# Optimization experiments

Measured on AMD Instinct MI355X. Metric: run time of the kernel, lower is better.

## Reference

```python
import jax, jax.numpy as jnp
import numpy as np

B, S, D_MODEL = 2, 2048, 1024
NUM_HEADS, ATTN_DIM = 16, 64


def setup_inputs() -> dict:
    key = jax.random.key(0)
    ks = jax.random.split(key, 9)
    scale = 1.0 / np.sqrt(D_MODEL)
    states = jax.random.normal(ks[0], (B, S, D_MODEL), dtype=jnp.float32)
    Wq = jax.random.normal(ks[1], (D_MODEL, NUM_HEADS * ATTN_DIM), dtype=jnp.float32) * scale
    bq = jnp.zeros((NUM_HEADS * ATTN_DIM,), dtype=jnp.float32)
    Wk = jax.random.normal(ks[2], (D_MODEL, NUM_HEADS * ATTN_DIM), dtype=jnp.float32) * scale
    bk = jnp.zeros((NUM_HEADS * ATTN_DIM,), dtype=jnp.float32)
    Wv = jax.random.normal(ks[3], (D_MODEL, NUM_HEADS * ATTN_DIM), dtype=jnp.float32) * scale
    bv = jnp.zeros((NUM_HEADS * ATTN_DIM,), dtype=jnp.float32)
    Wo = jax.random.normal(ks[4], (NUM_HEADS * ATTN_DIM, D_MODEL), dtype=jnp.float32) * scale
    bo = jnp.zeros((D_MODEL,), dtype=jnp.float32)
    return {"states": states, "Wq": Wq, "bq": bq, "Wk": Wk, "bk": bk,
            "Wv": Wv, "bv": bv, "Wo": Wo, "bo": bo}


def reference(states, Wq, bq, Wk, bk, Wv, bv, Wo, bo):
    b, s, _ = states.shape
    h, d = NUM_HEADS, ATTN_DIM

    def proj(W, bias):
        # tanh-activated Dense, then split heads: [b, s, h*d] -> [b, h, s, d]
        y = jnp.tanh(states @ W + bias)
        return y.reshape(b, s, h, d).transpose(0, 2, 1, 3)

    q, k, v = proj(Wq, bq), proj(Wk, bk), proj(Wv, bv)
    # scores: [b, h, s, s]
    alpha = jnp.einsum("bhqd,bhkd->bhqk", q, k) / jnp.sqrt(jnp.float32(d))
    # causal mask (row i attends to cols 0..i); masked logits set to float32.min
    causal = jnp.tril(jnp.ones((s, s), dtype=bool))
    alpha = jnp.where(causal, alpha, jnp.finfo(jnp.float32).min)
    alpha = jax.nn.softmax(alpha, axis=-1)
    ctx = jnp.einsum("bhqk,bhkd->bhqd", alpha, v)  # [b, h, s, d]
    ctx = ctx.transpose(0, 2, 1, 3).reshape(b, s, h * d)
    return jnp.tanh(ctx @ Wo + bo)
```

## Files before the change

kernel.cpp:

```cpp
#include <hip/hip_runtime.h>
#include <math.h>

typedef unsigned short u16;
typedef __attribute__((ext_vector_type(4))) float f32x4;
typedef __attribute__((ext_vector_type(16))) float f32x16;
typedef __attribute__((ext_vector_type(8))) short bf16x8;

#define B_ 2
#define S_ 2048
#define DM 1024
#define H_ 16
#define AD 64
#define ME 4194304
#define SC 0.18033688011112042f
#define SMAX 12.0f

#define GLL(g, s) __builtin_amdgcn_global_load_lds( \
  (const __attribute__((address_space(1))) void*)(g), \
  (__attribute__((address_space(3))) void*)(s), 16, 0, 0)

__device__ inline u16 f2bf(float f) {
  union { float f; unsigned u; } v; v.f = f;
  unsigned r = v.u + 0x7fffu + ((v.u >> 16) & 1u);
  return (u16)(r >> 16);
}

__device__ inline unsigned cvt_pk_bf16(float lo, float hi) {
  unsigned r;
  asm("v_cvt_pk_bf16_f32 %0, %1, %2" : "=v"(r) : "v"(lo), "v"(hi));
  return r;
}

__global__ __launch_bounds__(256) void conv_states(const float* __restrict__ in,
                                                   u16* __restrict__ out) {
  int i = (blockIdx.x * 256 + threadIdx.x) * 8;
  const float4* p = (const float4*)(in + i);
  float4 a = p[0], b = p[1];
  bf16x8 o;
  o[0] = (short)f2bf(a.x); o[1] = (short)f2bf(a.y);
  o[2] = (short)f2bf(a.z); o[3] = (short)f2bf(a.w);
  o[4] = (short)f2bf(b.x); o[5] = (short)f2bf(b.y);
  o[6] = (short)f2bf(b.z); o[7] = (short)f2bf(b.w);
  *(bf16x8*)&out[i] = o;
}

__global__ void transpose_w(const float* __restrict__ Wq, const float* __restrict__ Wk,
                            const float* __restrict__ Wv, const float* __restrict__ Wo,
                            u16* __restrict__ Wt) {
  __shared__ float t[32][33];
  int z = blockIdx.z;
  const float* W = (z == 0) ? Wq : (z == 1) ? Wk : (z == 2) ? Wv : Wo;
  u16* out = Wt + (size_t)z * DM * DM;
  int n0 = blockIdx.x * 32, k0 = blockIdx.y * 32;
  int tx = threadIdx.x, ty = threadIdx.y;
  t[ty][tx] = W[(k0 + ty) * DM + n0 + tx];
  __syncthreads();
  out[(n0 + ty) * DM + k0 + tx] = f2bf(t[tx][ty]);
}

__global__ __launch_bounds__(256) void qkv_gemm(
    const u16* __restrict__ A, const u16* __restrict__ Wt,
    const float* __restrict__ bq, const float* __restrict__ bk, const float* __restrict__ bv,
    u16* __restrict__ Qw, u16* __restrict__ Kw, u16* __restrict__ Vtw) {
  __shared__ __attribute__((aligned(16))) u16 lA[128 * 32];
  __shared__ __attribute__((aligned(16))) u16 lB[128 * 32];
  const int z = blockIdx.z;
  const u16* Bt = Wt + (size_t)z * DM * DM;
  const int m0 = blockIdx.y * 128, n0 = blockIdx.x * 128;
  const int tid = threadIdx.x;
  const int wid = tid >> 6, l = tid & 63;
  const int lr = l & 15, lk = l >> 4;
  const int wm = (wid >> 1) * 64, wn = (wid & 1) * 64;
  const int srow = wid * 32 + (l >> 2);
  const int scol = (l & 3) * 8;

  f32x4 acc[4][4] = {};

  for (int k0 = 0; k0 < DM; k0 += 32) {
    const u16* gA = &A[(size_t)(m0 + srow) * DM + k0 + scol];
    const u16* gB = &Bt[(size_t)(n0 + srow) * DM + k0 + scol];
    GLL(gA,           lA + wid * 1024);
    GLL(gA + 16 * DM, lA + wid * 1024 + 512);
    GLL(gB,           lB + wid * 1024);
    GLL(gB + 16 * DM, lB + wid * 1024 + 512);
    __syncthreads();
    bf16x8 af[4], bfr[4];
#pragma unroll
    for (int g = 0; g < 4; ++g) {
      af[g]  = *(const bf16x8*)&lA[(wm + g * 16 + lr) * 32 + lk * 8];
      bfr[g] = *(const bf16x8*)&lB[(wn + g * 16 + lr) * 32 + lk * 8];
    }
#pragma unroll
    for (int mg = 0; mg < 4; ++mg)
#pragma unroll
      for (int ng = 0; ng < 4; ++ng)
        acc[mg][ng] = __builtin_amdgcn_mfma_f32_16x16x32_bf16(af[mg], bfr[ng], acc[mg][ng], 0, 0, 0);
    __syncthreads();
  }

  const float* bias = (z == 0) ? bq : (z == 1) ? bk : bv;
#pragma unroll
  for (int mg = 0; mg < 4; ++mg)
#pragma unroll
    for (int ng = 0; ng < 4; ++ng)
#pragma unroll
      for (int r = 0; r < 4; ++r) {
        int m = m0 + wm + mg * 16 + lk * 4 + r;
        int n = n0 + wn + ng * 16 + lr;
        float v = tanhf(acc[mg][ng][r] + bias[n]);
        if (z == 0) v *= SC;
        u16 h16 = f2bf(v);
        int bb = m >> 11, s = m & 2047, hh = n >> 6, d = n & 63;
        if (z == 2) Vtw[((size_t)(bb * H_ + hh) * AD + d) * S_ + s] = h16;
        else ((z == 0) ? Qw : Kw)[((size_t)(bb * H_ + hh) * S_ + s) * AD + d] = h16;
      }
}

__global__ __launch_bounds__(256) void out_gemm(
    const u16* __restrict__ A, const u16* __restrict__ Bt,
    const float* __restrict__ bo, float* __restrict__ out) {
  __shared__ __attribute__((aligned(16))) u16 lA[128 * 32];
  __shared__ __attribute__((aligned(16))) u16 lB[128 * 32];
  const int m0 = blockIdx.y * 128, n0 = blockIdx.x * 128;
  const int tid = threadIdx.x;
  const int wid = tid >> 6, l = tid & 63;
  const int lr = l & 15, lk = l >> 4;
  const int wm = (wid >> 1) * 64, wn = (wid & 1) * 64;
  const int srow = wid * 32 + (l >> 2);
  const int scol = (l & 3) * 8;

  f32x4 acc[4][4] = {};

  for (int k0 = 0; k0 < DM; k0 += 32) {
    const u16* gA = &A[(size_t)(m0 + srow) * DM + k0 + scol];
    const u16* gB = &Bt[(size_t)(n0 + srow) * DM + k0 + scol];
    GLL(gA,           lA + wid * 1024);
    GLL(gA + 16 * DM, lA + wid * 1024 + 512);
    GLL(gB,           lB + wid * 1024);
    GLL(gB + 16 * DM, lB + wid * 1024 + 512);
    __syncthreads();
    bf16x8 af[4], bfr[4];
#pragma unroll
    for (int g = 0; g < 4; ++g) {
      af[g]  = *(const bf16x8*)&lA[(wm + g * 16 + lr) * 32 + lk * 8];
      bfr[g] = *(const bf16x8*)&lB[(wn + g * 16 + lr) * 32 + lk * 8];
    }
#pragma unroll
    for (int mg = 0; mg < 4; ++mg)
#pragma unroll
      for (int ng = 0; ng < 4; ++ng)
        acc[mg][ng] = __builtin_amdgcn_mfma_f32_16x16x32_bf16(af[mg], bfr[ng], acc[mg][ng], 0, 0, 0);
    __syncthreads();
  }

#pragma unroll
  for (int mg = 0; mg < 4; ++mg)
#pragma unroll
    for (int ng = 0; ng < 4; ++ng)
#pragma unroll
      for (int r = 0; r < 4; ++r) {
        int m = m0 + wm + mg * 16 + lk * 4 + r;
        int n = n0 + wn + ng * 16 + lr;
        out[(size_t)m * DM + n] = tanhf(acc[mg][ng][r] + bo[n]);
      }
}

__global__ __launch_bounds__(256, 2) void attn_kernel(
    const u16* __restrict__ Q, const u16* __restrict__ K,
    const u16* __restrict__ Vt, float* __restrict__ O0, float* __restrict__ O1,
    float* __restrict__ L0, float* __restrict__ L1) {
  __shared__ __attribute__((aligned(16))) char smem[65536];
  const int u = blockIdx.x >> 5;
  const int bh = blockIdx.x & 31;
  int t, lo;
  if (u < 9)       { t = 7 + u; lo = 0; }
  else if (u == 9) { t = 15;    lo = 8; }
  else { int k = u - 10; int sz = 7 - (k >> 1);
         if (k & 1) { t = sz + 7; lo = 8; } else { t = sz - 1; lo = 0; } }
  const int khi = lo ? t : (t < 7 ? t : 7);

  const int tid = threadIdx.x, wl = tid >> 6, l = tid & 63;
  const int lq = l & 31, hl = l >> 5;
  const int q0 = t * 128 + wl * 32;

  const char* Qb = (const char*)(Q + (size_t)bh * S_ * AD);
  const char* Kb = (const char*)(K + (size_t)bh * S_ * AD);
  const char* Vb = (const char*)(Vt + (size_t)bh * AD * S_);

  int kcst[4], vcst[4], ldso[4];
#pragma unroll
  for (int i = 0; i < 4; ++i) {
    int c = wl * 4 + i;
    int o = c * 1024 + l * 16;
    ldso[i] = c * 1024;
    int row = o >> 8;
    int un = (o & 255) ^ ((row & 15) << 4);
    kcst[i] = (row * 2 + (un >> 7)) * 128 + (un & 127);
    vcst[i] = row * (2 * S_) + un;
  }

  bf16x8 qf[4];
#pragma unroll
  for (int ds = 0; ds < 4; ++ds)
    qf[ds] = *(const bf16x8*)(Qb + (size_t)(q0 + lq) * 128 + ds * 32 + hl * 16);

  f32x16 accO[2] = {};
  float lsum = 0.f;

#pragma unroll
  for (int i = 0; i < 4; ++i) {
    GLL(Kb + lo * 16384 + kcst[i], smem + ldso[i]);
    GLL(Vb + lo * 256  + vcst[i], smem + 32768 + ldso[i]);
  }
  asm volatile("s_waitcnt vmcnt(0)" ::: "memory");
  __syncthreads();

  for (int kb = lo; kb <= khi; ++kb) {
    const int buf = (kb - lo) & 1;
    if (kb < khi) {
      const int nb = kb + 1, nbuf = buf ^ 1;
#pragma unroll
      for (int i = 0; i < 4; ++i) {
        GLL(Kb + nb * 16384 + kcst[i], smem + nbuf * 16384 + ldso[i]);
        GLL(Vb + nb * 256  + vcst[i], smem + 32768 + nbuf * 16384 + ldso[i]);
      }
    }

    const char* kl = smem + buf * 16384;
    const char* vl = smem + 32768 + buf * 16384;
    const bool diag = (kb == t);
    const int wlim = diag ? wl : 3;

    for (int s = 0; s <= wlim; ++s) {
      f32x16 c = {};
      const int kvl = s * 32 + lq;
      const int rp = kvl >> 1, kbit = kvl & 1;
      const int swz = (rp & 15) << 4;
      __builtin_amdgcn_s_setprio(1);
#pragma unroll
      for (int ds = 0; ds < 4; ++ds) {
        bf16x8 a = *(const bf16x8*)(kl + rp * 256 +
                     (((kbit << 7) | (ds * 32 + hl * 16)) ^ swz));
        c = __builtin_amdgcn_mfma_f32_32x32x16_bf16(a, qf[ds], c, 0, 0, 0);
      }
      __builtin_amdgcn_s_setprio(0);

      const bool tri = diag && (s == wl);
#pragma unroll
      for (int r = 0; r < 16; ++r) {
        float e = __builtin_amdgcn_exp2f(c[r] - SMAX);
        if (tri) {
          int kc = (r & 3) + 8 * (r >> 2) + 4 * hl;
          if (kc > lq) e = 0.f;
        }
        c[r] = e;
        lsum += e;
      }

      unsigned uu[8], su[8];
#pragma unroll
      for (int i = 0; i < 8; ++i) {
        uu[i] = cvt_pk_bf16(c[2 * i], c[2 * i + 1]);
        su[i] = (unsigned)__shfl_xor((int)uu[i], 32);
      }
      union { unsigned w[4]; bf16x8 v; } c0, c1;
      c0.w[0] = hl ? su[2] : uu[0]; c0.w[1] = hl ? su[3] : uu[1];
      c0.w[2] = hl ? uu[2] : su[0]; c0.w[3] = hl ? uu[3] : su[1];
      c1.w[0] = hl ? su[6] : uu[4]; c1.w[1] = hl ? su[7] : uu[5];
      c1.w[2] = hl ? uu[6] : su[4]; c1.w[3] = hl ? uu[7] : su[5];

      __builtin_amdgcn_s_setprio(1);
#pragma unroll
      for (int d = 0; d < 2; ++d) {
        const int drow = d * 32 + lq;
        const int vswz = (drow & 15) << 4;
        bf16x8 a0 = *(const bf16x8*)(vl + drow * 256 + ((s * 64 + hl * 16) ^ vswz));
        bf16x8 a1 = *(const bf16x8*)(vl + drow * 256 + ((s * 64 + 32 + hl * 16) ^ vswz));
        accO[d] = __builtin_amdgcn_mfma_f32_32x32x16_bf16(a0, c0.v, accO[d], 0, 0, 0);
        accO[d] = __builtin_amdgcn_mfma_f32_32x32x16_bf16(a1, c1.v, accO[d], 0, 0, 0);
      }
      __builtin_amdgcn_s_setprio(0);
    }

    asm volatile("s_waitcnt vmcnt(0)" ::: "memory");
    __syncthreads();
  }

  lsum += __shfl_xor(lsum, 32);
  const int q = q0 + lq;
  float* Ob = lo ? O1 + ((size_t)bh * 1024 + (q - 1024)) * 64
                 : O0 + ((size_t)bh * 2048 + q) * 64;
#pragma unroll
  for (int d = 0; d < 2; ++d)
#pragma unroll
    for (int g = 0; g < 4; ++g) {
      f32x4 w;
      w[0] = accO[d][4 * g];     w[1] = accO[d][4 * g + 1];
      w[2] = accO[d][4 * g + 2]; w[3] = accO[d][4 * g + 3];
      *(f32x4*)&Ob[d * 32 + 8 * g + 4 * hl] = w;
    }
  if (!hl) {
    if (lo) L1[(size_t)bh * 1024 + (q - 1024)] = lsum;
    else    L0[(size_t)bh * 2048 + q] = lsum;
  }
}

__global__ __launch_bounds__(256) void attn_norm(
    const float* __restrict__ O0, const float* __restrict__ O1,
    const float* __restrict__ L0, const float* __restrict__ L1,
    u16* __restrict__ ctx) {
  const int tid = threadIdx.x;
  const int row = blockIdx.x * 64 + (tid >> 2);
  const int sub = tid & 3;
  const int bh = row >> 11, q = row & 2047;
  float lv = L0[row];
  const f32x4* p0 = (const f32x4*)(O0 + (size_t)row * 64 + sub * 16);
  f32x4 v0 = p0[0], v1 = p0[1], v2 = p0[2], v3 = p0[3];
  if (q >= 1024) {
    size_t r1 = (size_t)bh * 1024 + (q - 1024);
    lv += L1[r1];
    const f32x4* p1 = (const f32x4*)(O1 + r1 * 64 + sub * 16);
    v0 += p1[0]; v1 += p1[1]; v2 += p1[2]; v3 += p1[3];
  }
  const float inv = 1.f / lv;
  const int b = bh >> 4, h = bh & 15;
  unsigned w[8];
  w[0] = cvt_pk_bf16(v0[0] * inv, v0[1] * inv);
  w[1] = cvt_pk_bf16(v0[2] * inv, v0[3] * inv);
  w[2] = cvt_pk_bf16(v1[0] * inv, v1[1] * inv);
  w[3] = cvt_pk_bf16(v1[2] * inv, v1[3] * inv);
  w[4] = cvt_pk_bf16(v2[0] * inv, v2[1] * inv);
  w[5] = cvt_pk_bf16(v2[2] * inv, v2[3] * inv);
  w[6] = cvt_pk_bf16(v3[0] * inv, v3[1] * inv);
  w[7] = cvt_pk_bf16(v3[2] * inv, v3[3] * inv);
  unsigned* dst = (unsigned*)(ctx + ((size_t)b * S_ + q) * DM + h * AD + sub * 16);
#pragma unroll
  for (int i = 0; i < 8; ++i) dst[i] = w[i];
}

extern "C" void kernel_launch(void* const* d_in, const int* in_sizes, int n_in,
                              void* d_out, int out_size, void* d_ws, size_t ws_size,
                              hipStream_t stream) {
  const float* states = (const float*)d_in[0];
  const float* Wq = (const float*)d_in[1];
  const float* bq = (const float*)d_in[2];
  const float* Wk = (const float*)d_in[3];
  const float* bk = (const float*)d_in[4];
  const float* Wv = (const float*)d_in[5];
  const float* bv = (const float*)d_in[6];
  const float* Wo = (const float*)d_in[7];
  const float* bo = (const float*)d_in[8];
  float* out = (float*)d_out;

  u16* sbf = (u16*)d_ws;
  u16* wt  = sbf + ME;
  u16* Qw  = wt + ME;
  u16* Kw  = Qw + ME;
  u16* Vtw = Kw + ME;
  u16* ctx = Vtw + ME;
  float* O0 = (float*)(ctx + ME);
  float* O1 = O0 + ME;
  float* L0 = O1 + ME / 2;
  float* L1 = L0 + B_ * H_ * S_;

  conv_states<<<ME / (256 * 8), 256, 0, stream>>>(states, sbf);
  transpose_w<<<dim3(32, 32, 4), dim3(32, 32), 0, stream>>>(Wq, Wk, Wv, Wo, wt);
  qkv_gemm<<<dim3(8, 32, 3), 256, 0, stream>>>(sbf, wt, bq, bk, bv, Qw, Kw, Vtw);
  attn_kernel<<<768, 256, 0, stream>>>(Qw, Kw, Vtw, O0, O1, L0, L1);
  attn_norm<<<1024, 256, 0, stream>>>(O0, O1, L0, L1, ctx);
  out_gemm<<<dim3(8, 32), 256, 0, stream>>>(ctx, wt + 3 * (size_t)DM * DM, bo, out);
}
```

Baseline: 132.4 us.

## Rewrite QKV GEMM as 256x256 tile, 8-wave, multi-buffered pipelined kernel

Replaces the 128x128 single-buffered QKV projection GEMM with a 512-thread kernel computing 256x256 tiles. The three weight matrices are treated as one concatenated N=3072 matrix, so the z grid dimension goes away. Global-to-LDS loads are issued through a multi-stage prefetch with swizzled shared-memory layout, partial vmcnt waits and raw barriers, and MFMA blocks are raised in priority. The aim is to overlap memory with MFMA and raise arithmetic intensity per tile. In exchange it uses 128KB of LDS, giving one block per CU, and only 192 blocks for a 256-CU device, which risks underfilling the GPU.

New measurement: 136.6 us. +3.2%, slower.

```diff
diff --git a/kernel.cpp b/kernel.cpp
--- a/kernel.cpp
+++ b/kernel.cpp
@@ -58,62 +58,114 @@
   out[(n0 + ty) * DM + k0 + tx] = f2bf(t[tx][ty]);
 }
 
-__global__ __launch_bounds__(256) void qkv_gemm(
+__global__ __launch_bounds__(512, 2) void qkv_gemm8(
     const u16* __restrict__ A, const u16* __restrict__ Wt,
     const float* __restrict__ bq, const float* __restrict__ bk, const float* __restrict__ bv,
     u16* __restrict__ Qw, u16* __restrict__ Kw, u16* __restrict__ Vtw) {
-  __shared__ __attribute__((aligned(16))) u16 lA[128 * 32];
-  __shared__ __attribute__((aligned(16))) u16 lB[128 * 32];
-  const int z = blockIdx.z;
-  const u16* Bt = Wt + (size_t)z * DM * DM;
-  const int m0 = blockIdx.y * 128, n0 = blockIdx.x * 128;
-  const int tid = threadIdx.x;
-  const int wid = tid >> 6, l = tid & 63;
+  __shared__ __attribute__((aligned(16))) char smem[131072];
+  const int n0 = blockIdx.x * 256;
+  const int m0 = blockIdx.y * 256;
+  const int tid = threadIdx.x, wid = tid >> 6, l = tid & 63;
   const int lr = l & 15, lk = l >> 4;
-  const int wm = (wid >> 1) * 64, wn = (wid & 1) * 64;
-  const int srow = wid * 32 + (l >> 2);
-  const int scol = (l & 3) * 8;
-
-  f32x4 acc[4][4] = {};
-
-  for (int k0 = 0; k0 < DM; k0 += 32) {
-    const u16* gA = &A[(size_t)(m0 + srow) * DM + k0 + scol];
-    const u16* gB = &Bt[(size_t)(n0 + srow) * DM + k0 + scol];
-    GLL(gA,           lA + wid * 1024);
-    GLL(gA + 16 * DM, lA + wid * 1024 + 512);
-    GLL(gB,           lB + wid * 1024);
-    GLL(gB + 16 * DM, lB + wid * 1024 + 512);
-    __syncthreads();
-    bf16x8 af[4], bfr[4];
-#pragma unroll
-    for (int g = 0; g < 4; ++g) {
-      af[g]  = *(const bf16x8*)&lA[(wm + g * 16 + lr) * 32 + lk * 8];
-      bfr[g] = *(const bf16x8*)&lB[(wn + g * 16 + lr) * 32 + lk * 8];
+  const int wr = wid >> 2, wc = wid & 3;
+
+  const int sidx = (l & 7) ^ (l >> 3);
+  const int row0 = wid * 16 + (l >> 3) * 2 + (sidx >> 2);
+  const int row1 = 128 + row0;
+  const int soff = (sidx & 3) * 16;
+  const char* Ab = (const char*)A;
+  const char* Bb = (const char*)Wt;
+  const size_t asrc0 = (size_t)(m0 + row0) * 2048 + soff;
+  const size_t asrc1 = (size_t)(m0 + row1) * 2048 + soff;
+  const size_t bsrc0 = (size_t)(n0 + row0) * 2048 + soff;
+  const size_t bsrc1 = (size_t)(n0 + row1) * 2048 + soff;
+  const int dwave = wid * 1024;
+
+  const int lnoff = (lr >> 1) * 128 + (((((lr & 1) << 2) | lk) ^ (lr >> 1)) << 4);
+
+  f32x4 acc[8][4] = {};
+
+#define STAGE_SET(SS, SKH, SBUF) do { \
+    const int kof_ = ((SS) * 64 + (SKH) * 32) * 2; \
+    char* da_ = smem + (SBUF) * 32768 + (SKH) * 16384 + dwave; \
+    char* db_ = da_ + 65536; \
+    GLL(Ab + asrc0 + kof_, da_); \
+    GLL(Ab + asrc1 + kof_, da_ + 8192); \
+    GLL(Bb + bsrc0 + kof_, db_); \
+    GLL(Bb + bsrc1 + kof_, db_ + 8192); \
+  } while (0)
+
+#define SP_PHASE(C, KH, SS, SKH, SBUF) do { \
+    const char* ab_ = smem + (C) * 32768 + (KH) * 16384; \
+    const char* bb_ = ab_ + 65536; \
+    bf16x8 af_[8], bf_[4]; \
+    _Pragma("unroll") \
+    for (int mf = 0; mf < 8; ++mf) \
+      af_[mf] = *(const bf16x8*)(ab_ + wr * 8192 + mf * 1024 + lnoff); \
+    _Pragma("unroll") \
+    for (int nf = 0; nf < 4; ++nf) \
+      bf_[nf] = *(const bf16x8*)(bb_ + wc * 4096 + nf * 1024 + lnoff); \
+    STAGE_SET(SS, SKH, SBUF); \
+    __builtin_amdgcn_s_setprio(1); \
+    _Pragma("unroll") \
+    for (int mf = 0; mf < 8; ++mf) \
+      _Pragma("unroll") \
+      for (int nf = 0; nf < 4; ++nf) \
+        acc[mf][nf] = __builtin_amdgcn_mfma_f32_16x16x32_bf16(af_[mf], bf_[nf], acc[mf][nf], 0, 0, 0); \
+    __builtin_amdgcn_s_setprio(0); \
+    asm volatile("s_waitcnt vmcnt(8)" ::: "memory"); \
+    __builtin_amdgcn_s_barrier(); \
+    asm volatile("" ::: "memory"); \
+  } while (0)
+
+  STAGE_SET(0, 0, 0);
+  STAGE_SET(0, 1, 0);
+  STAGE_SET(1, 0, 1);
+  asm volatile("s_waitcnt vmcnt(8)" ::: "memory");
+  __builtin_amdgcn_s_barrier();
+  asm volatile("" ::: "memory");
+
+#pragma unroll 2
+  for (int t = 0; t < 16; ++t) {
+    const int c = t & 1;
+    const int s1 = (t + 1 < 16) ? t + 1 : 15;
+    const int s2 = (t + 2 < 16) ? t + 2 : 15;
+    SP_PHASE(c, 0, s1, 1, c ^ 1);
+    SP_PHASE(c, 1, s2, 0, c);
+  }
+#undef SP_PHASE
+#undef STAGE_SET
+
+  const int z = n0 >> 10;
+  const float* bias = (z == 0) ? bq : (z == 1) ? bk : bv;
+#pragma unroll
+  for (int mf = 0; mf < 8; ++mf) {
+    const int m = m0 + wr * 128 + mf * 16 + lk * 4;
+    const int bb = m >> 11, s = m & 2047;
+#pragma unroll
+    for (int nf = 0; nf < 4; ++nf) {
+      const int n = n0 + wc * 64 + nf * 16 + lr;
+      const int nn = n & 1023;
+      const int hh = nn >> 6, d = nn & 63;
+      const float bv_ = bias[nn];
+      float v0 = tanhf(acc[mf][nf][0] + bv_);
+      float v1 = tanhf(acc[mf][nf][1] + bv_);
+      float v2 = tanhf(acc[mf][nf][2] + bv_);
+      float v3 = tanhf(acc[mf][nf][3] + bv_);
+      if (z == 0) { v0 *= SC; v1 *= SC; v2 *= SC; v3 *= SC; }
+      if (z == 2) {
+        ushort4 pk;
+        pk.x = f2bf(v0); pk.y = f2bf(v1); pk.z = f2bf(v2); pk.w = f2bf(v3);
+        *(ushort4*)&Vtw[((size_t)(bb * H_ + hh) * AD + d) * S_ + s] = pk;
+      } else {
+        u16* dst = ((z == 0) ? Qw : Kw) + ((size_t)(bb * H_ + hh) * S_ + s) * AD + d;
+        dst[0]      = f2bf(v0);
+        dst[AD]     = f2bf(v1);
+        dst[2 * AD] = f2bf(v2);
+        dst[3 * AD] = f2bf(v3);
+      }
     }
-#pragma unroll
-    for (int mg = 0; mg < 4; ++mg)
-#pragma unroll
-      for (int ng = 0; ng < 4; ++ng)
-        acc[mg][ng] = __builtin_amdgcn_mfma_f32_16x16x32_bf16(af[mg], bfr[ng], acc[mg][ng], 0, 0, 0);
-    __syncthreads();
-  }
-
-  const float* bias = (z == 0) ? bq : (z == 1) ? bk : bv;
-#pragma unroll
-  for (int mg = 0; mg < 4; ++mg)
-#pragma unroll
-    for (int ng = 0; ng < 4; ++ng)
-#pragma unroll
-      for (int r = 0; r < 4; ++r) {
-        int m = m0 + wm + mg * 16 + lk * 4 + r;
-        int n = n0 + wn + ng * 16 + lr;
-        float v = tanhf(acc[mg][ng][r] + bias[n]);
-        if (z == 0) v *= SC;
-        u16 h16 = f2bf(v);
-        int bb = m >> 11, s = m & 2047, hh = n >> 6, d = n & 63;
-        if (z == 2) Vtw[((size_t)(bb * H_ + hh) * AD + d) * S_ + s] = h16;
-        else ((z == 0) ? Qw : Kw)[((size_t)(bb * H_ + hh) * S_ + s) * AD + d] = h16;
-      }
+  }
 }
 
 __global__ __launch_bounds__(256) void out_gemm(
@@ -365,7 +417,7 @@
 
   conv_states<<<ME / (256 * 8), 256, 0, stream>>>(states, sbf);
   transpose_w<<<dim3(32, 32, 4), dim3(32, 32), 0, stream>>>(Wq, Wk, Wv, Wo, wt);
-  qkv_gemm<<<dim3(8, 32, 3), 256, 0, stream>>>(sbf, wt, bq, bk, bv, Qw, Kw, Vtw);
+  qkv_gemm8<<<dim3(12, 16), 512, 0, stream>>>(sbf, wt, bq, bk, bv, Qw, Kw, Vtw);
   attn_kernel<<<768, 256, 0, stream>>>(Qw, Kw, Vtw, O0, O1, L0, L1);
   attn_norm<<<1024, 256, 0, stream>>>(O0, O1, L0, L1, ctx);
   out_gemm<<<dim3(8, 32), 256, 0, stream>>>(ctx, wt + 3 * (size_t)DM * DM, bo, out);
```

## Split causal attention KV range into three chunks with register-staged single-buffer LDS

Applied to the files above, without the earlier changes.

Reworks the attention work split so each query tile's KV range is divided into up to three chunks of six key blocks instead of two of eight, giving 960 blocks. Short tiles write normalized bf16 context directly and skip the merge. It replaces async global-to-LDS double buffering with register prefetch into a single 32KB LDS buffer, which allows three blocks per CU. The risks are extra partial-output traffic, an added barrier per iteration, and higher register pressure. O2/L2 partials also reuse the workspace region that holds the converted states.

Result: no change. 130.7 us (-1.3%).

```diff
diff --git a/kernel.cpp b/kernel.cpp
--- a/kernel.cpp
+++ b/kernel.cpp
@@ -165,19 +165,24 @@
       }
 }
 
-__global__ __launch_bounds__(256, 2) void attn_kernel(
+__global__ __launch_bounds__(256, 3) void attn_kernel(
     const u16* __restrict__ Q, const u16* __restrict__ K,
-    const u16* __restrict__ Vt, float* __restrict__ O0, float* __restrict__ O1,
-    float* __restrict__ L0, float* __restrict__ L1) {
-  __shared__ __attribute__((aligned(16))) char smem[65536];
+    const u16* __restrict__ Vt, u16* __restrict__ ctx,
+    float* __restrict__ O0, float* __restrict__ O1, float* __restrict__ O2,
+    float* __restrict__ L0, float* __restrict__ L1, float* __restrict__ L2) {
+  __shared__ __attribute__((aligned(16))) char smem[32768];
   const int u = blockIdx.x >> 5;
   const int bh = blockIdx.x & 31;
   int t, lo;
-  if (u < 9)       { t = 7 + u; lo = 0; }
-  else if (u == 9) { t = 15;    lo = 8; }
-  else { int k = u - 10; int sz = 7 - (k >> 1);
-         if (k & 1) { t = sz + 7; lo = 8; } else { t = sz - 1; lo = 0; } }
-  const int khi = lo ? t : (t < 7 ? t : 7);
+  if (u < 11)       { t = u + 5;  lo = 0; }
+  else if (u < 16)  { t = u;      lo = 6; }
+  else if (u == 16) { t = 4;      lo = 0; }
+  else if (u == 17) { t = 10;     lo = 6; }
+  else { int r = u - 18, g = r / 3, c = r % 3;
+         if (c == 0)      { t = 3 - g;  lo = 0; }
+         else if (c == 1) { t = 9 - g;  lo = 6; }
+         else             { t = 15 - g; lo = 12; } }
+  const int hi = (lo == 0) ? (t < 5 ? t : 5) : ((lo == 6) ? (t < 11 ? t : 11) : t);
 
   const int tid = threadIdx.x, wl = tid >> 6, l = tid & 63;
   const int lq = l & 31, hl = l >> 5;
@@ -192,7 +197,7 @@
   for (int i = 0; i < 4; ++i) {
     int c = wl * 4 + i;
     int o = c * 1024 + l * 16;
-    ldso[i] = c * 1024;
+    ldso[i] = c * 1024 + l * 16;
     int row = o >> 8;
     int un = (o & 255) ^ ((row & 15) << 4);
     kcst[i] = (row * 2 + (un >> 7)) * 128 + (un & 127);
@@ -207,27 +212,35 @@
   f32x16 accO[2] = {};
   float lsum = 0.f;
 
-#pragma unroll
-  for (int i = 0; i < 4; ++i) {
-    GLL(Kb + lo * 16384 + kcst[i], smem + ldso[i]);
-    GLL(Vb + lo * 256  + vcst[i], smem + 32768 + ldso[i]);
-  }
-  asm volatile("s_waitcnt vmcnt(0)" ::: "memory");
+  {
+    bf16x8 kr[4], vr[4];
+#pragma unroll
+    for (int i = 0; i < 4; ++i) {
+      kr[i] = *(const bf16x8*)(Kb + (size_t)lo * 16384 + kcst[i]);
+      vr[i] = *(const bf16x8*)(Vb + (size_t)lo * 256  + vcst[i]);
+    }
+#pragma unroll
+    for (int i = 0; i < 4; ++i) {
+      *(bf16x8*)(smem + ldso[i])         = kr[i];
+      *(bf16x8*)(smem + 16384 + ldso[i]) = vr[i];
+    }
+  }
   __syncthreads();
 
-  for (int kb = lo; kb <= khi; ++kb) {
-    const int buf = (kb - lo) & 1;
-    if (kb < khi) {
-      const int nb = kb + 1, nbuf = buf ^ 1;
+  const char* kl = smem;
+  const char* vl = smem + 16384;
+
+  for (int kb = lo; kb <= hi; ++kb) {
+    bf16x8 krn[4], vrn[4];
+    const bool pf = (kb < hi);
+    if (pf) {
 #pragma unroll
       for (int i = 0; i < 4; ++i) {
-        GLL(Kb + nb * 16384 + kcst[i], smem + nbuf * 16384 + ldso[i]);
-        GLL(Vb + nb * 256  + vcst[i], smem + 32768 + nbuf * 16384 + ldso[i]);
-      }
-    }
-
-    const char* kl = smem + buf * 16384;
-    const char* vl = smem + 32768 + buf * 16384;
+        krn[i] = *(const bf16x8*)(Kb + (size_t)(kb + 1) * 16384 + kcst[i]);
+        vrn[i] = *(const bf16x8*)(Vb + (size_t)(kb + 1) * 256  + vcst[i]);
+      }
+    }
+
     const bool diag = (kb == t);
     const int wlim = diag ? wl : 3;
 
@@ -263,11 +276,11 @@
         uu[i] = cvt_pk_bf16(c[2 * i], c[2 * i + 1]);
         su[i] = (unsigned)__shfl_xor((int)uu[i], 32);
       }
-      union { unsigned w[4]; bf16x8 v; } c0, c1;
-      c0.w[0] = hl ? su[2] : uu[0]; c0.w[1] = hl ? su[3] : uu[1];
-      c0.w[2] = hl ? uu[2] : su[0]; c0.w[3] = hl ? uu[3] : su[1];
-      c1.w[0] = hl ? su[6] : uu[4]; c1.w[1] = hl ? su[7] : uu[5];
-      c1.w[2] = hl ? uu[6] : su[4]; c1.w[3] = hl ? uu[7] : su[5];
+      union { unsigned w[4]; bf16x8 v; } c0_, c1_;
+      c0_.w[0] = hl ? su[2] : uu[0]; c0_.w[1] = hl ? su[3] : uu[1];
+      c0_.w[2] = hl ? uu[2] : su[0]; c0_.w[3] = hl ? uu[3] : su[1];
+      c1_.w[0] = hl ? su[6] : uu[4]; c1_.w[1] = hl ? su[7] : uu[5];
+      c1_.w[2] = hl ? uu[6] : su[4]; c1_.w[3] = hl ? uu[7] : su[5];
 
       __builtin_amdgcn_s_setprio(1);
 #pragma unroll
@@ -276,51 +289,76 @@
         const int vswz = (drow & 15) << 4;
         bf16x8 a0 = *(const bf16x8*)(vl + drow * 256 + ((s * 64 + hl * 16) ^ vswz));
         bf16x8 a1 = *(const bf16x8*)(vl + drow * 256 + ((s * 64 + 32 + hl * 16) ^ vswz));
-        accO[d] = __builtin_amdgcn_mfma_f32_32x32x16_bf16(a0, c0.v, accO[d], 0, 0, 0);
-        accO[d] = __builtin_amdgcn_mfma_f32_32x32x16_bf16(a1, c1.v, accO[d], 0, 0, 0);
+        accO[d] = __builtin_amdgcn_mfma_f32_32x32x16_bf16(a0, c0_.v, accO[d], 0, 0, 0);
+        accO[d] = __builtin_amdgcn_mfma_f32_32x32x16_bf16(a1, c1_.v, accO[d], 0, 0, 0);
       }
       __builtin_amdgcn_s_setprio(0);
     }
 
-    asm volatile("s_waitcnt vmcnt(0)" ::: "memory");
+    __syncthreads();
+    if (pf) {
+#pragma unroll
+      for (int i = 0; i < 4; ++i) {
+        *(bf16x8*)(smem + ldso[i])         = krn[i];
+        *(bf16x8*)(smem + 16384 + ldso[i]) = vrn[i];
+      }
+    }
     __syncthreads();
   }
 
   lsum += __shfl_xor(lsum, 32);
   const int q = q0 + lq;
-  float* Ob = lo ? O1 + ((size_t)bh * 1024 + (q - 1024)) * 64
-                 : O0 + ((size_t)bh * 2048 + q) * 64;
-#pragma unroll
-  for (int d = 0; d < 2; ++d)
-#pragma unroll
-    for (int g = 0; g < 4; ++g) {
-      f32x4 w;
-      w[0] = accO[d][4 * g];     w[1] = accO[d][4 * g + 1];
-      w[2] = accO[d][4 * g + 2]; w[3] = accO[d][4 * g + 3];
-      *(f32x4*)&Ob[d * 32 + 8 * g + 4 * hl] = w;
-    }
-  if (!hl) {
-    if (lo) L1[(size_t)bh * 1024 + (q - 1024)] = lsum;
-    else    L0[(size_t)bh * 2048 + q] = lsum;
+
+  if (lo == 0 && t < 6) {
+    const float inv = 1.f / lsum;
+    u16* cb_ = ctx + ((size_t)(bh >> 4) * S_ + q) * DM + (bh & 15) * AD;
+#pragma unroll
+    for (int d = 0; d < 2; ++d)
+#pragma unroll
+      for (int g = 0; g < 4; ++g) {
+        unsigned w0 = cvt_pk_bf16(accO[d][4 * g] * inv,     accO[d][4 * g + 1] * inv);
+        unsigned w1 = cvt_pk_bf16(accO[d][4 * g + 2] * inv, accO[d][4 * g + 3] * inv);
+        unsigned* dst = (unsigned*)(cb_ + d * 32 + 8 * g + 4 * hl);
+        dst[0] = w0; dst[1] = w1;
+      }
+  } else {
+    float* Ob; float* Lb;
+    if (lo == 0)      { size_t r = (size_t)bh * 1280 + (q - 768);  Ob = O0 + r * 64; Lb = L0 + r; }
+    else if (lo == 6) { size_t r = (size_t)bh * 1280 + (q - 768);  Ob = O1 + r * 64; Lb = L1 + r; }
+    else              { size_t r = (size_t)bh * 512  + (q - 1536); Ob = O2 + r * 64; Lb = L2 + r; }
+#pragma unroll
+    for (int d = 0; d < 2; ++d)
+#pragma unroll
+      for (int g = 0; g < 4; ++g) {
+        f32x4 w;
+        w[0] = accO[d][4 * g];     w[1] = accO[d][4 * g + 1];
+        w[2] = accO[d][4 * g + 2]; w[3] = accO[d][4 * g + 3];
+        *(f32x4*)&Ob[d * 32 + 8 * g + 4 * hl] = w;
+      }
+    if (!hl) *Lb = lsum;
   }
 }
 
 __global__ __launch_bounds__(256) void attn_norm(
     const float* __restrict__ O0, const float* __restrict__ O1,
-    const float* __restrict__ L0, const float* __restrict__ L1,
+    const float* __restrict__ O2, const float* __restrict__ L0,
+    const float* __restrict__ L1, const float* __restrict__ L2,
     u16* __restrict__ ctx) {
   const int tid = threadIdx.x;
-  const int row = blockIdx.x * 64 + (tid >> 2);
+  const int rowl = blockIdx.x * 64 + (tid >> 2);
   const int sub = tid & 3;
-  const int bh = row >> 11, q = row & 2047;
-  float lv = L0[row];
-  const f32x4* p0 = (const f32x4*)(O0 + (size_t)row * 64 + sub * 16);
-  f32x4 v0 = p0[0], v1 = p0[1], v2 = p0[2], v3 = p0[3];
-  if (q >= 1024) {
-    size_t r1 = (size_t)bh * 1024 + (q - 1024);
-    lv += L1[r1];
-    const f32x4* p1 = (const f32x4*)(O1 + r1 * 64 + sub * 16);
-    v0 += p1[0]; v1 += p1[1]; v2 += p1[2]; v3 += p1[3];
+  const int bh = rowl / 1280, qr = rowl - bh * 1280;
+  const int q = 768 + qr;
+  float lv = L0[rowl] + L1[rowl];
+  const f32x4* p0 = (const f32x4*)(O0 + (size_t)rowl * 64 + sub * 16);
+  const f32x4* p1 = (const f32x4*)(O1 + (size_t)rowl * 64 + sub * 16);
+  f32x4 v0 = p0[0] + p1[0], v1 = p0[1] + p1[1];
+  f32x4 v2 = p0[2] + p1[2], v3 = p0[3] + p1[3];
+  if (q >= 1536) {
+    size_t r2 = (size_t)bh * 512 + (q - 1536);
+    lv += L2[r2];
+    const f32x4* p2 = (const f32x4*)(O2 + r2 * 64 + sub * 16);
+    v0 += p2[0]; v1 += p2[1]; v2 += p2[2]; v3 += p2[3];
   }
   const float inv = 1.f / lv;
   const int b = bh >> 4, h = bh & 15;
@@ -359,14 +397,16 @@
   u16* Vtw = Kw + ME;
   u16* ctx = Vtw + ME;
   float* O0 = (float*)(ctx + ME);
-  float* O1 = O0 + ME;
-  float* L0 = O1 + ME / 2;
-  float* L1 = L0 + B_ * H_ * S_;
+  float* O1 = O0 + (size_t)32 * 1280 * 64;
+  float* O2 = (float*)d_ws;
+  float* L0 = O2 + (size_t)32 * 512 * 64;
+  float* L1 = L0 + 32 * 1280;
+  float* L2 = L1 + 32 * 1280;
 
   conv_states<<<ME / (256 * 8), 256, 0, stream>>>(states, sbf);
   transpose_w<<<dim3(32, 32, 4), dim3(32, 32), 0, stream>>>(Wq, Wk, Wv, Wo, wt);
   qkv_gemm<<<dim3(8, 32, 3), 256, 0, stream>>>(sbf, wt, bq, bk, bv, Qw, Kw, Vtw);
-  attn_kernel<<<768, 256, 0, stream>>>(Qw, Kw, Vtw, O0, O1, L0, L1);
-  attn_norm<<<1024, 256, 0, stream>>>(O0, O1, L0, L1, ctx);
+  attn_kernel<<<960, 256, 0, stream>>>(Qw, Kw, Vtw, ctx, O0, O1, O2, L0, L1, L2);
+  attn_norm<<<640, 256, 0, stream>>>(O0, O1, O2, L0, L1, L2, ctx);
   out_gemm<<<dim3(8, 32), 256, 0, stream>>>(ctx, wt + 3 * (size_t)DM * DM, bo, out);
 }
```
